# Kernel optimization log

Measured on AMD Instinct MI355X. Metric: run time of the kernel, lower is better.

## Reference

```python
import jax, jax.numpy as jnp
import numpy as np

B, S, D, H, DFF = 4, 2048, 1024, 16, 4096
DK = D // H
EPS = 1e-6


def setup_inputs() -> dict:
    key = jax.random.key(0)
    ks = jax.random.split(key, 8)
    s = 0.02
    return {
        "x": jax.random.normal(ks[0], (B, S, D), jnp.float32),
        "src_mask": jnp.ones((B, 1, 1, S), jnp.int32),
        "w_q": jax.random.normal(ks[1], (D, D), jnp.float32) * s,
        "w_k": jax.random.normal(ks[2], (D, D), jnp.float32) * s,
        "w_v": jax.random.normal(ks[3], (D, D), jnp.float32) * s,
        "w_o": jax.random.normal(ks[4], (D, D), jnp.float32) * s,
        "w1": jax.random.normal(ks[5], (DFF, D), jnp.float32) * s,
        "b1": jnp.zeros((DFF,), jnp.float32),
        "w2": jax.random.normal(ks[6], (D, DFF), jnp.float32) * s,
        "b2": jnp.zeros((D,), jnp.float32),
        "gamma1": jnp.ones((1,), jnp.float32),
        "beta1": jnp.zeros((1,), jnp.float32),
        "gamma2": jnp.ones((1,), jnp.float32),
        "beta2": jnp.zeros((1,), jnp.float32),
    }


def layernorm(x, gamma, beta):
    # matches torch source: unbiased std (ddof=1), eps added to std, scalar gamma/beta
    mean = jnp.mean(x, axis=-1, keepdims=True)
    std = jnp.std(x, axis=-1, keepdims=True, ddof=1)
    return gamma * (x - mean) / (std + EPS) + beta


def mha(x, w_q, w_k, w_v, w_o):
    # Linear(bias=False): y = x @ W.T
    q = (x @ w_q.T).reshape(B, S, H, DK).transpose(0, 2, 1, 3)  # [B,H,S,DK]
    k = (x @ w_k.T).reshape(B, S, H, DK).transpose(0, 2, 1, 3)
    v = (x @ w_v.T).reshape(B, S, H, DK).transpose(0, 2, 1, 3)
    scores = jnp.einsum('bhqd,bhkd->bhqk', q, k) / np.float32(np.sqrt(DK))
    # NOTE: source calls attention.masked_fill(...) without assigning the result,
    # so the mask has no effect; faithfully replicated (mask unused).
    attn = jax.nn.softmax(scores, axis=-1)
    ctx = jnp.einsum('bhqk,bhkd->bhqd', attn, v)  # [B,H,S,DK]
    ctx = ctx.transpose(0, 2, 1, 3).reshape(B, S, D)
    return ctx @ w_o.T


def ffn(x, w1, b1, w2, b2):
    return jax.nn.relu(x @ w1.T + b1) @ w2.T + b2


def reference(x, src_mask, w_q, w_k, w_v, w_o, w1, b1, w2, b2,
              gamma1, beta1, gamma2, beta2):
    # pre-norm residual blocks; dropout is identity in eval
    x = x + mha(layernorm(x, gamma1, beta1), w_q, w_k, w_v, w_o)
    x = x + ffn(layernorm(x, gamma2, beta2), w1, b1, w2, b2)
    return x
```

## Files before the change

kernel.cpp:

```cpp
#include <hip/hip_runtime.h>
#include <hip/hip_bf16.h>

#define DEV static __device__ __forceinline__

typedef unsigned short u16;
typedef float fp32x4 __attribute__((ext_vector_type(4)));
typedef short bf16x8 __attribute__((ext_vector_type(8)));
typedef short bf16x4 __attribute__((ext_vector_type(4)));

DEV float bf2f(u16 u) { return __uint_as_float(((unsigned)u) << 16); }
DEV u16 f2bf(float f) {
  unsigned x = __float_as_uint(f);
  x += 0x7fffu + ((x >> 16) & 1u);
  return (u16)(x >> 16);
}

DEV unsigned cvt_pk_bf16(float a, float b) {
  unsigned r;
  asm("v_cvt_pk_bf16_f32 %0, %1, %2" : "=v"(r) : "v"(a), "v"(b));
  return r;
}

DEV void gload_lds16(const void* g, void* l) {
  __builtin_amdgcn_global_load_lds(
      (__attribute__((address_space(1))) void*)(unsigned long long)g,
      (__attribute__((address_space(3))) void*)(unsigned int)(unsigned long long)l,
      16, 0, 0);
}

__global__ __launch_bounds__(256) void cvt_kernel(const float* __restrict__ in,
                                                  u16* __restrict__ out) {
  const int i = blockIdx.x * 256 + threadIdx.x;
  const fp32x4 v = ((const fp32x4*)in)[i];
  bf16x4 o;
#pragma unroll
  for (int j = 0; j < 4; j++) o[j] = (short)f2bf(v[j]);
  ((bf16x4*)out)[i] = o;
}

__global__ __launch_bounds__(256) void ln_kernel(const float* __restrict__ x,
                                                 u16* __restrict__ y,
                                                 const float* __restrict__ gamma,
                                                 const float* __restrict__ beta) {
  const int row = blockIdx.x;
  const int t = threadIdx.x;
  const fp32x4 v = ((const fp32x4*)(x + (size_t)row * 1024))[t];
  float s = v[0] + v[1] + v[2] + v[3];
  float ss = v[0] * v[0] + v[1] * v[1] + v[2] * v[2] + v[3] * v[3];
#pragma unroll
  for (int o = 32; o > 0; o >>= 1) {
    s += __shfl_down(s, o);
    ss += __shfl_down(ss, o);
  }
  __shared__ float rs[4], rss[4];
  const int w = t >> 6;
  if ((t & 63) == 0) { rs[w] = s; rss[w] = ss; }
  __syncthreads();
  const float S = rs[0] + rs[1] + rs[2] + rs[3];
  const float SS = rss[0] + rss[1] + rss[2] + rss[3];
  const float mean = S * (1.0f / 1024.0f);
  const float var = fmaxf((SS - 1024.0f * mean * mean) * (1.0f / 1023.0f), 0.0f);
  const float sc = gamma[0] / (sqrtf(var) + 1e-6f);
  const float be = beta[0];
  bf16x4 o;
#pragma unroll
  for (int j = 0; j < 4; j++) o[j] = (short)f2bf((v[j] - mean) * sc + be);
  ((bf16x4*)(y + (size_t)row * 1024))[t] = o;
}

template <int EPI>
__global__ __launch_bounds__(256, 2) void gemm_bt(
    const u16* __restrict__ A, const u16* __restrict__ W, u16* __restrict__ Cb,
    float* __restrict__ Cf, const float* __restrict__ bias,
    const float* __restrict__ resid, int M, int N, int K,
    u16* __restrict__ CbK, u16* __restrict__ CbV) {
  __shared__ u16 sA[128 * 32];
  __shared__ u16 sB[128 * 32];
  const int t = threadIdx.x;
  const int lane = t & 63;
  const int w = t >> 6;
  const int wr = (w >> 1) * 64;
  const int wc = (w & 1) * 64;
  const int lr = lane & 15;
  const int hi = lane >> 4;

  const int nwgx = gridDim.x;
  const int orig = blockIdx.y * nwgx + blockIdx.x;
  const int cpx = (nwgx * gridDim.y) >> 3;
  const int logical = (orig & 7) * cpx + (orig >> 3);
  const int bx = logical % nwgx, by = logical / nwgx;

  const u16* gA = A + (size_t)(by * 128 + (t >> 2)) * K + (t & 3) * 8;
  const u16* gB = W + (size_t)(bx * 128 + (t >> 2)) * K + (t & 3) * 8;
  const size_t rstep = (size_t)64 * K;
  u16* lA = &sA[t * 8];
  u16* lB = &sB[t * 8];

  const fp32x4 zero4 = {0.f, 0.f, 0.f, 0.f};
  fp32x4 acc[4][4];
#pragma unroll
  for (int i = 0; i < 4; i++)
#pragma unroll
    for (int j = 0; j < 4; j++) acc[i][j] = zero4;

  for (int k0 = 0; k0 < K; k0 += 32) {
    gload_lds16(gA, lA);
    gload_lds16(gA + rstep, lA + 2048);
    gload_lds16(gB, lB);
    gload_lds16(gB + rstep, lB + 2048);
    gA += 32;
    gB += 32;
    __syncthreads();
    bf16x8 af[4], bfr[4];
#pragma unroll
    for (int i = 0; i < 4; i++)
      af[i] = *(const bf16x8*)&sA[(wr + i * 16 + lr) * 32 + hi * 8];
#pragma unroll
    for (int j = 0; j < 4; j++)
      bfr[j] = *(const bf16x8*)&sB[(wc + j * 16 + lr) * 32 + hi * 8];
#pragma unroll
    for (int i = 0; i < 4; i++)
#pragma unroll
      for (int j = 0; j < 4; j++)
        acc[i][j] =
            __builtin_amdgcn_mfma_f32_16x16x32_bf16(af[i], bfr[j], acc[i][j], 0, 0, 0);
    __syncthreads();
  }

  const int row0 = by * 128 + wr + hi * 4;
  const int col0 = bx * 128 + wc + lr;
  float bj[4] = {0.f, 0.f, 0.f, 0.f};
  if (EPI == 1 || EPI == 3) {
#pragma unroll
    for (int j = 0; j < 4; j++) bj[j] = bias[col0 + j * 16];
  }
  u16* qkvDst = nullptr;
  int colL0 = 0;
  if (EPI == 4) {
    const int sel = col0 >> 10;
    qkvDst = (sel == 0) ? Cb : (sel == 1 ? CbK : CbV);
    colL0 = col0 & 1023;
  }
#pragma unroll
  for (int i = 0; i < 4; i++) {
#pragma unroll
    for (int r = 0; r < 4; r++) {
      const size_t row = (size_t)(row0 + i * 16 + r);
#pragma unroll
      for (int j = 0; j < 4; j++) {
        float v = acc[i][j][r];
        if (EPI == 4) {
          qkvDst[row * 1024 + colL0 + j * 16] = f2bf(v);
          continue;
        }
        const int col = col0 + j * 16;
        if (EPI == 1) v = fmaxf(v + bj[j], 0.f);
        if (EPI == 3) v += bj[j];
        if (EPI >= 2) {
          v += resid[row * N + col];
          Cf[row * N + col] = v;
        } else {
          Cb[row * N + col] = f2bf(v);
        }
      }
    }
  }
}

__global__ __launch_bounds__(256) void vtrans_kernel(const u16* __restrict__ V,
                                                     u16* __restrict__ VT) {
  const int st = blockIdx.x;
  const int h = blockIdx.y;
  const int b = blockIdx.z;
  const int t = threadIdx.x;
  const int r = t >> 2, c0 = (t & 3) * 16;
  __shared__ u16 sT[64][72];

  const u16* src = V + ((size_t)(b * 2048 + st * 64 + r)) * 1024 + h * 64 + c0;
  bf16x8 v0 = *(const bf16x8*)src;
  bf16x8 v1 = *(const bf16x8*)(src + 8);
  const int cb = c0 ^ ((r >> 4) << 4);
  *(bf16x8*)&sT[r][cb] = v0;
  *(bf16x8*)&sT[r][cb + 8] = v1;
  __syncthreads();

  const int dc = r ^ ((c0 >> 4) << 4);
  bf16x8 o0, o1;
#pragma unroll
  for (int i = 0; i < 8; i++) o0[i] = sT[c0 + i][dc];
#pragma unroll
  for (int i = 0; i < 8; i++) o1[i] = sT[c0 + 8 + i][dc];
  u16* dst = VT + ((size_t)((b * 16 + h) * 64 + r)) * 2048 + st * 64 + c0;
  *(bf16x8*)dst = o0;
  *(bf16x8*)(dst + 8) = o1;
}

DEV int swz(int row, int chunk) { return row * 64 + ((chunk ^ (row & 7)) << 3); }

__global__ __launch_bounds__(256, 2) void attn_kernel(const u16* __restrict__ Q,
                                                      const u16* __restrict__ K,
                                                      const u16* __restrict__ VT,
                                                      u16* __restrict__ O) {
  const int orig = blockIdx.x + 32 * (blockIdx.y + 16 * blockIdx.z);
  const int logical = (orig & 7) * 256 + (orig >> 3);
  const int qt = logical & 31;
  const int h = (logical >> 5) & 15;
  const int b = logical >> 9;

  const int t = threadIdx.x, lane = t & 63, w = t >> 6;
  const int lr = lane & 15, hi = lane >> 4;

  __shared__ u16 sK[64 * 64];
  __shared__ u16 sVT[64 * 64];
  __shared__ u16 sQP[64 * 64];

  const size_t base = ((size_t)b * 2048) * 1024 + (size_t)h * 64;
  const size_t vbase = (((size_t)b * 16 + h) * 64) * 2048;
  const int r = t >> 2, c0 = (t & 3) * 16;
  const int wch = (t & 3) * 2;

  {
    const float qs = 0.125f * 1.44269504f;
    const u16* src = Q + base + (size_t)(qt * 64 + r) * 1024 + c0;
    bf16x8 u0 = *(const bf16x8*)src;
    bf16x8 u1 = *(const bf16x8*)(src + 8);
    union { unsigned u[4]; bf16x8 v; } q0, q1;
#pragma unroll
    for (int j = 0; j < 4; j++)
      q0.u[j] = cvt_pk_bf16(bf2f((u16)u0[2 * j]) * qs, bf2f((u16)u0[2 * j + 1]) * qs);
#pragma unroll
    for (int j = 0; j < 4; j++)
      q1.u[j] = cvt_pk_bf16(bf2f((u16)u1[2 * j]) * qs, bf2f((u16)u1[2 * j + 1]) * qs);
    *(bf16x8*)&sQP[swz(r, wch)] = q0.v;
    *(bf16x8*)&sQP[swz(r, wch + 1)] = q1.v;
  }
  __syncthreads();
  const int qrow = w * 16 + lr;
  bf16x8 qreg0 = *(const bf16x8*)&sQP[swz(qrow, hi)];
  bf16x8 qreg1 = *(const bf16x8*)&sQP[swz(qrow, 4 + hi)];

  bf16x8 kA, kB, vA, vB;
  {
    const u16* ks = K + base + (size_t)r * 1024 + c0;
    kA = *(const bf16x8*)ks;
    kB = *(const bf16x8*)(ks + 8);
    const u16* vs = VT + vbase + (size_t)r * 2048 + c0;
    vA = *(const bf16x8*)vs;
    vB = *(const bf16x8*)(vs + 8);
  }

  const fp32x4 zero4 = {0.f, 0.f, 0.f, 0.f};
  fp32x4 onT[4];
#pragma unroll
  for (int df = 0; df < 4; df++) onT[df] = zero4;
  float mrun = -1e30f, lrun = 0.f;

  for (int kt = 0; kt < 32; ++kt) {
    __syncthreads();
    *(bf16x8*)&sK[swz(r, wch)] = kA;
    *(bf16x8*)&sK[swz(r, wch + 1)] = kB;
    *(bf16x8*)&sVT[swz(r, wch)] = vA;
    *(bf16x8*)&sVT[swz(r, wch + 1)] = vB;
    __syncthreads();
    if (kt < 31) {
      const u16* kn = K + base + (size_t)((kt + 1) * 64 + r) * 1024 + c0;
      kA = *(const bf16x8*)kn;
      kB = *(const bf16x8*)(kn + 8);
      const u16* vn = VT + vbase + (size_t)r * 2048 + (kt + 1) * 64 + c0;
      vA = *(const bf16x8*)vn;
      vB = *(const bf16x8*)(vn + 8);
    }

    fp32x4 sc[4];
    __builtin_amdgcn_s_setprio(1);
#pragma unroll
    for (int kk = 0; kk < 4; kk++) {
      fp32x4 a = zero4;
      bf16x8 kf0 = *(const bf16x8*)&sK[swz(kk * 16 + lr, hi)];
      bf16x8 kf1 = *(const bf16x8*)&sK[swz(kk * 16 + lr, 4 + hi)];
      a = __builtin_amdgcn_mfma_f32_16x16x32_bf16(kf0, qreg0, a, 0, 0, 0);
      a = __builtin_amdgcn_mfma_f32_16x16x32_bf16(kf1, qreg1, a, 0, 0, 0);
      sc[kk] = a;
    }
    __builtin_amdgcn_s_setprio(0);

    float m0 = fmaxf(fmaxf(sc[0][0], sc[0][1]), fmaxf(sc[0][2], sc[0][3]));
    float m1 = fmaxf(fmaxf(sc[1][0], sc[1][1]), fmaxf(sc[1][2], sc[1][3]));
    float m2 = fmaxf(fmaxf(sc[2][0], sc[2][1]), fmaxf(sc[2][2], sc[2][3]));
    float m3 = fmaxf(fmaxf(sc[3][0], sc[3][1]), fmaxf(sc[3][2], sc[3][3]));
    float mloc = fmaxf(fmaxf(m0, m1), fmaxf(m2, m3));
    mloc = fmaxf(mloc, __shfl_xor(mloc, 16));
    mloc = fmaxf(mloc, __shfl_xor(mloc, 32));
    if (!__all(mloc - mrun <= 11.0f)) {
      const float mnew = fmaxf(mrun, mloc);
      const float alpha = exp2f(mrun - mnew);
      lrun *= alpha;
#pragma unroll
      for (int df = 0; df < 4; df++) onT[df] *= alpha;
      mrun = mnew;
    }
#pragma unroll
    for (int kk = 0; kk < 4; kk++) {
      float p0 = exp2f(sc[kk][0] - mrun), p1 = exp2f(sc[kk][1] - mrun);
      float p2 = exp2f(sc[kk][2] - mrun), p3 = exp2f(sc[kk][3] - mrun);
      lrun += (p0 + p1) + (p2 + p3);
      uint2 pk = {cvt_pk_bf16(p0, p1), cvt_pk_bf16(p2, p3)};
      *(uint2*)&sQP[swz(qrow, 2 * kk + (hi >> 1)) + (hi & 1) * 4] = pk;
    }

    __builtin_amdgcn_s_setprio(1);
#pragma unroll
    for (int df = 0; df < 4; df++) {
#pragma unroll
      for (int ks = 0; ks < 2; ks++) {
        bf16x8 vf = *(const bf16x8*)&sVT[swz(df * 16 + lr, ks * 4 + hi)];
        bf16x8 pf = *(const bf16x8*)&sQP[swz(qrow, ks * 4 + hi)];
        onT[df] = __builtin_amdgcn_mfma_f32_16x16x32_bf16(vf, pf, onT[df], 0, 0, 0);
      }
    }
    __builtin_amdgcn_s_setprio(0);
  }

  lrun += __shfl_xor(lrun, 16);
  lrun += __shfl_xor(lrun, 32);
  const float invl = 1.0f / lrun;
  u16* dst = O + base + (size_t)(qt * 64 + qrow) * 1024;
#pragma unroll
  for (int df = 0; df < 4; df++) {
    uint2 o2 = {cvt_pk_bf16(onT[df][0] * invl, onT[df][1] * invl),
                cvt_pk_bf16(onT[df][2] * invl, onT[df][3] * invl)};
    *(uint2*)&dst[df * 16 + hi * 4] = o2;
  }
}

extern "C" void kernel_launch(void* const* d_in, const int* in_sizes, int n_in,
                              void* d_out, int out_size, void* d_ws, size_t ws_size,
                              hipStream_t stream) {
  const float* x = (const float*)d_in[0];
  const float* wq = (const float*)d_in[2];
  const float* wk = (const float*)d_in[3];
  const float* wv = (const float*)d_in[4];
  const float* wo = (const float*)d_in[5];
  const float* w1 = (const float*)d_in[6];
  const float* b1 = (const float*)d_in[7];
  const float* w2 = (const float*)d_in[8];
  const float* b2 = (const float*)d_in[9];
  const float* g1 = (const float*)d_in[10];
  const float* be1 = (const float*)d_in[11];
  const float* g2 = (const float*)d_in[12];
  const float* be2 = (const float*)d_in[13];
  float* out = (float*)d_out;

  const size_t MB = 1024ull * 1024ull;
  char* ws = (char*)d_ws;
  if (ws_size < 136 * MB) return;

  u16* wqkv = (u16*)(ws + 0 * MB);
  u16* wqb = (u16*)(ws + 0 * MB);
  u16* wkb = (u16*)(ws + 2 * MB);
  u16* wvb = (u16*)(ws + 4 * MB);
  u16* wob = (u16*)(ws + 6 * MB);
  u16* w1b = (u16*)(ws + 8 * MB);
  u16* w2b = (u16*)(ws + 16 * MB);
  u16* Qb = (u16*)(ws + 24 * MB);
  u16* Kb = (u16*)(ws + 40 * MB);
  u16* Vb = (u16*)(ws + 56 * MB);
  u16* Ctx = (u16*)(ws + 72 * MB);
  u16* Hb = (u16*)(ws + 24 * MB);
  u16* Yb = (u16*)(ws + 88 * MB);
  u16* VTb = (u16*)(ws + 88 * MB);
  float* X2 = (float*)(ws + 104 * MB);

  dim3 blk(256);

  cvt_kernel<<<1024, blk, 0, stream>>>(wq, wqb);
  cvt_kernel<<<1024, blk, 0, stream>>>(wk, wkb);
  cvt_kernel<<<1024, blk, 0, stream>>>(wv, wvb);
  cvt_kernel<<<1024, blk, 0, stream>>>(wo, wob);
  cvt_kernel<<<4096, blk, 0, stream>>>(w1, w1b);
  cvt_kernel<<<4096, blk, 0, stream>>>(w2, w2b);

  ln_kernel<<<8192, blk, 0, stream>>>(x, Yb, g1, be1);

  gemm_bt<4><<<dim3(24, 64), blk, 0, stream>>>(Yb, wqkv, Qb, nullptr, nullptr, nullptr,
                                               8192, 3072, 1024, Kb, Vb);
  vtrans_kernel<<<dim3(32, 16, 4), blk, 0, stream>>>(Vb, VTb);

  attn_kernel<<<dim3(32, 16, 4), blk, 0, stream>>>(Qb, Kb, VTb, Ctx);

  gemm_bt<2><<<dim3(8, 64), blk, 0, stream>>>(Ctx, wob, nullptr, X2, nullptr, x, 8192,
                                              1024, 1024, nullptr, nullptr);

  ln_kernel<<<8192, blk, 0, stream>>>(X2, Yb, g2, be2);

  gemm_bt<1><<<dim3(32, 64), blk, 0, stream>>>(Yb, w1b, Hb, nullptr, b1, nullptr, 8192,
                                               4096, 1024, nullptr, nullptr);

  gemm_bt<3><<<dim3(8, 64), blk, 0, stream>>>(Hb, w2b, nullptr, out, b2, X2, 8192, 1024,
                                              4096, nullptr, nullptr);
}
```

Baseline: 451.2 us.

## Add 256x256 triple-buffered GEMM kernel for QKV and FFN1 projections

Measured after the change: 464.3 us. 2.9% more time.

```diff
diff --git a/kernel.cpp b/kernel.cpp
--- a/kernel.cpp
+++ b/kernel.cpp
@@ -72,8 +72,7 @@
 __global__ __launch_bounds__(256, 2) void gemm_bt(
     const u16* __restrict__ A, const u16* __restrict__ W, u16* __restrict__ Cb,
     float* __restrict__ Cf, const float* __restrict__ bias,
-    const float* __restrict__ resid, int M, int N, int K,
-    u16* __restrict__ CbK, u16* __restrict__ CbV) {
+    const float* __restrict__ resid, int M, int N, int K) {
   __shared__ u16 sA[128 * 32];
   __shared__ u16 sB[128 * 32];
   const int t = threadIdx.x;
@@ -134,13 +133,6 @@
 #pragma unroll
     for (int j = 0; j < 4; j++) bj[j] = bias[col0 + j * 16];
   }
-  u16* qkvDst = nullptr;
-  int colL0 = 0;
-  if (EPI == 4) {
-    const int sel = col0 >> 10;
-    qkvDst = (sel == 0) ? Cb : (sel == 1 ? CbK : CbV);
-    colL0 = col0 & 1023;
-  }
 #pragma unroll
   for (int i = 0; i < 4; i++) {
 #pragma unroll
@@ -148,12 +140,8 @@
       const size_t row = (size_t)(row0 + i * 16 + r);
 #pragma unroll
       for (int j = 0; j < 4; j++) {
+        const int col = col0 + j * 16;
         float v = acc[i][j][r];
-        if (EPI == 4) {
-          qkvDst[row * 1024 + colL0 + j * 16] = f2bf(v);
-          continue;
-        }
-        const int col = col0 + j * 16;
         if (EPI == 1) v = fmaxf(v + bj[j], 0.f);
         if (EPI == 3) v += bj[j];
         if (EPI >= 2) {
@@ -165,6 +153,129 @@
       }
     }
   }
+}
+
+template <int EPI>
+__global__ __launch_bounds__(512, 1) void gemm256(
+    const u16* __restrict__ A, const u16* __restrict__ W, u16* __restrict__ C0,
+    u16* __restrict__ C1, u16* __restrict__ C2, const float* __restrict__ bias,
+    int N, int K) {
+  __shared__ __attribute__((aligned(16))) u16 sA[3][256 * 32];
+  __shared__ __attribute__((aligned(16))) u16 sB[3][256 * 32];
+  const int t = threadIdx.x;
+  const int l = t & 63, wid = t >> 6;
+  const int lr = l & 15, hi = l >> 4;
+  const int wm = wid >> 2, wn = wid & 3;
+
+  const int nwgx = gridDim.x;
+  const int orig = blockIdx.y * nwgx + blockIdx.x;
+  const int cpx = (nwgx * gridDim.y) >> 3;
+  const int logical = (orig & 7) * cpx + (orig >> 3);
+  const int bn = logical % nwgx, bm = logical / nwgx;
+
+  const int rl = l >> 2;
+  const int srcsw = (l & 3) ^ ((l >> 2) & 3) ^ ((l >> 4) & 3);
+  const int rb0 = wid * 16, rb1 = 128 + wid * 16;
+  const u16* gA0 = A + (size_t)(bm * 256 + rb0 + rl) * K + srcsw * 8;
+  const u16* gA1 = A + (size_t)(bm * 256 + rb1 + rl) * K + srcsw * 8;
+  const u16* gB0 = W + (size_t)(bn * 256 + rb0 + rl) * K + srcsw * 8;
+  const u16* gB1 = W + (size_t)(bn * 256 + rb1 + rl) * K + srcsw * 8;
+
+#define STAGE_A(buf, ts)                                      \
+  gload_lds16(gA0 + (ts) * 32, &sA[buf][rb0 * 32 + l * 8]);   \
+  gload_lds16(gA1 + (ts) * 32, &sA[buf][rb1 * 32 + l * 8]);
+#define STAGE_B(buf, ts)                                      \
+  gload_lds16(gB0 + (ts) * 32, &sB[buf][rb0 * 32 + l * 8]);   \
+  gload_lds16(gB1 + (ts) * 32, &sB[buf][rb1 * 32 + l * 8]);
+
+  const int fsw = hi ^ ((lr ^ (lr >> 2)) & 3);
+
+  fp32x4 acc[8][4];
+  const fp32x4 zero4 = {0.f, 0.f, 0.f, 0.f};
+#pragma unroll
+  for (int m = 0; m < 8; m++)
+#pragma unroll
+    for (int n = 0; n < 4; n++) acc[m][n] = zero4;
+
+  STAGE_A(0, 0); STAGE_B(0, 0);
+  STAGE_A(1, 1); STAGE_B(1, 1);
+
+  const int nt = K / 32;
+  for (int tt = 0; tt < nt; ++tt) {
+    const int cur = tt % 3;
+    const int nxt = (tt + 2) % 3;
+    const int ts = (tt + 2) & (nt - 1);
+    asm volatile("s_waitcnt vmcnt(4)" ::: "memory");
+    __builtin_amdgcn_s_barrier();
+
+    bf16x8 bfrag[4], afrag[4];
+#pragma unroll
+    for (int n = 0; n < 4; n++)
+      bfrag[n] = *(const bf16x8*)&sB[cur][(wn * 64 + n * 16 + lr) * 32 + fsw * 8];
+#pragma unroll
+    for (int m = 0; m < 4; m++)
+      afrag[m] = *(const bf16x8*)&sA[cur][(wm * 128 + m * 16 + lr) * 32 + fsw * 8];
+    STAGE_A(nxt, ts);
+    __builtin_amdgcn_s_barrier();
+    __builtin_amdgcn_s_setprio(1);
+#pragma unroll
+    for (int m = 0; m < 4; m++)
+#pragma unroll
+      for (int n = 0; n < 4; n++)
+        acc[m][n] =
+            __builtin_amdgcn_mfma_f32_16x16x32_bf16(afrag[m], bfrag[n], acc[m][n], 0, 0, 0);
+    __builtin_amdgcn_s_setprio(0);
+
+#pragma unroll
+    for (int m = 0; m < 4; m++)
+      afrag[m] =
+          *(const bf16x8*)&sA[cur][(wm * 128 + 64 + m * 16 + lr) * 32 + fsw * 8];
+    STAGE_B(nxt, ts);
+    __builtin_amdgcn_s_barrier();
+    __builtin_amdgcn_s_setprio(1);
+#pragma unroll
+    for (int m = 0; m < 4; m++)
+#pragma unroll
+      for (int n = 0; n < 4; n++)
+        acc[4 + m][n] = __builtin_amdgcn_mfma_f32_16x16x32_bf16(afrag[m], bfrag[n],
+                                                                acc[4 + m][n], 0, 0, 0);
+    __builtin_amdgcn_s_setprio(0);
+  }
+  asm volatile("s_waitcnt vmcnt(0)" ::: "memory");
+
+  const int row0 = bm * 256 + wm * 128 + hi * 4;
+  const int col0 = bn * 256 + wn * 64 + lr;
+  float bj[4] = {0.f, 0.f, 0.f, 0.f};
+  if (EPI == 1) {
+#pragma unroll
+    for (int n = 0; n < 4; n++) bj[n] = bias[col0 + n * 16];
+  }
+  u16* qkvDst = C0;
+  int colL0 = col0;
+  if (EPI == 4) {
+    const int sel = bn >> 2;
+    qkvDst = (sel == 0) ? C0 : (sel == 1 ? C1 : C2);
+    colL0 = col0 & 1023;
+  }
+#pragma unroll
+  for (int m = 0; m < 8; m++) {
+#pragma unroll
+    for (int rr = 0; rr < 4; rr++) {
+      const size_t row = (size_t)(row0 + m * 16 + rr);
+#pragma unroll
+      for (int n = 0; n < 4; n++) {
+        float v = acc[m][n][rr];
+        if (EPI == 1) {
+          v = fmaxf(v + bj[n], 0.f);
+          C0[row * N + col0 + n * 16] = f2bf(v);
+        } else {
+          qkvDst[row * 1024 + colL0 + n * 16] = f2bf(v);
+        }
+      }
+    }
+  }
+#undef STAGE_A
+#undef STAGE_B
 }
 
 __global__ __launch_bounds__(256) void vtrans_kernel(const u16* __restrict__ V,
@@ -382,20 +493,20 @@
 
   ln_kernel<<<8192, blk, 0, stream>>>(x, Yb, g1, be1);
 
-  gemm_bt<4><<<dim3(24, 64), blk, 0, stream>>>(Yb, wqkv, Qb, nullptr, nullptr, nullptr,
-                                               8192, 3072, 1024, Kb, Vb);
+  gemm256<4><<<dim3(12, 32), dim3(512), 0, stream>>>(Yb, wqkv, Qb, Kb, Vb, nullptr,
+                                                     3072, 1024);
   vtrans_kernel<<<dim3(32, 16, 4), blk, 0, stream>>>(Vb, VTb);
 
   attn_kernel<<<dim3(32, 16, 4), blk, 0, stream>>>(Qb, Kb, VTb, Ctx);
 
   gemm_bt<2><<<dim3(8, 64), blk, 0, stream>>>(Ctx, wob, nullptr, X2, nullptr, x, 8192,
-                                              1024, 1024, nullptr, nullptr);
+                                              1024, 1024);
 
   ln_kernel<<<8192, blk, 0, stream>>>(X2, Yb, g2, be2);
 
-  gemm_bt<1><<<dim3(32, 64), blk, 0, stream>>>(Yb, w1b, Hb, nullptr, b1, nullptr, 8192,
-                                               4096, 1024, nullptr, nullptr);
+  gemm256<1><<<dim3(16, 32), dim3(512), 0, stream>>>(Yb, w1b, Hb, nullptr, nullptr, b1,
+                                                     4096, 1024);
 
   gemm_bt<3><<<dim3(8, 64), blk, 0, stream>>>(Hb, w2b, nullptr, out, b2, X2, 8192, 1024,
-                                              4096, nullptr, nullptr);
-}
+                                              4096);
+}
```

## Fuse V transpose into QKV GEMM epilogue and merge weight conversions

Applied to the files above, without the earlier changes.

Measured after the change: 440.3 us (median of 2 runs). -2.4%, faster.

```diff
diff --git a/kernel.cpp b/kernel.cpp
--- a/kernel.cpp
+++ b/kernel.cpp
@@ -28,14 +28,27 @@
       16, 0, 0);
 }
 
-__global__ __launch_bounds__(256) void cvt_kernel(const float* __restrict__ in,
-                                                  u16* __restrict__ out) {
-  const int i = blockIdx.x * 256 + threadIdx.x;
-  const fp32x4 v = ((const fp32x4*)in)[i];
+__global__ __launch_bounds__(256) void cvt_all(
+    const float* __restrict__ wq, const float* __restrict__ wk,
+    const float* __restrict__ wv, const float* __restrict__ wo,
+    const float* __restrict__ w1, const float* __restrict__ w2,
+    u16* __restrict__ dst) {
+  const size_t i = (size_t)blockIdx.x * 256 + threadIdx.x;
+  const size_t e = i * 4;
+  const float* src;
+  size_t off;
+  const size_t M1 = 1u << 20;
+  if (e < M1) { src = wq; off = e; }
+  else if (e < 2 * M1) { src = wk; off = e - M1; }
+  else if (e < 3 * M1) { src = wv; off = e - 2 * M1; }
+  else if (e < 4 * M1) { src = wo; off = e - 3 * M1; }
+  else if (e < 8 * M1) { src = w1; off = e - 4 * M1; }
+  else { src = w2; off = e - 8 * M1; }
+  const fp32x4 v = *(const fp32x4*)(src + off);
   bf16x4 o;
 #pragma unroll
   for (int j = 0; j < 4; j++) o[j] = (short)f2bf(v[j]);
-  ((bf16x4*)out)[i] = o;
+  ((bf16x4*)dst)[i] = o;
 }
 
 __global__ __launch_bounds__(256) void ln_kernel(const float* __restrict__ x,
@@ -129,18 +142,66 @@
 
   const int row0 = by * 128 + wr + hi * 4;
   const int col0 = bx * 128 + wc + lr;
+
+  if constexpr (EPI == 4) {
+    if (col0 < 2048) {
+      u16* qkvDst = (col0 >> 10) ? CbK : Cb;
+      const int colL0 = col0 & 1023;
+#pragma unroll
+      for (int i = 0; i < 4; i++)
+#pragma unroll
+        for (int r = 0; r < 4; r++) {
+          const size_t row = (size_t)(row0 + i * 16 + r);
+#pragma unroll
+          for (int j = 0; j < 4; j++)
+            qkvDst[row * 1024 + colL0 + j * 16] = f2bf(acc[i][j][r]);
+        }
+    } else {
+      __shared__ __attribute__((aligned(16))) u16 sT[2][64 * 72];
+#pragma unroll
+      for (int ph = 0; ph < 2; ++ph) {
+        __syncthreads();
+        if ((w >> 1) == ph) {
+          u16* R = sT[w & 1];
+#pragma unroll
+          for (int j = 0; j < 4; j++) {
+            const int ci = j * 16 + lr;
+            const int X = (ci ^ (ci >> 3)) & 7;
+#pragma unroll
+            for (int i = 0; i < 4; i++)
+#pragma unroll
+              for (int r = 0; r < 4; r++) {
+                const int ri = i * 16 + hi * 4 + r;
+                R[ci * 72 + ((((ri >> 3) ^ X) << 3) | (ri & 7))] =
+                    f2bf(acc[i][j][r]);
+              }
+          }
+        }
+        __syncthreads();
+        if ((w >> 1) == ph) {
+          const u16* R = sT[w & 1];
+          const int ci = lane;
+          const int X = (ci ^ (ci >> 3)) & 7;
+          const int h = (bx - 16) * 2 + (w & 1);
+          const int bidx = by >> 4;
+          const int sb_base = (by & 15) * 128 + (w >> 1) * 64;
+          u16* vdst = CbV + ((size_t)((bidx * 16 + h) * 64 + ci)) * 2048 + sb_base;
+#pragma unroll
+          for (int ch = 0; ch < 8; ch++) {
+            bf16x8 vv = *(const bf16x8*)&R[ci * 72 + ((ch ^ X) << 3)];
+            *(bf16x8*)(vdst + ch * 8) = vv;
+          }
+        }
+      }
+    }
+    return;
+  }
+
   float bj[4] = {0.f, 0.f, 0.f, 0.f};
   if (EPI == 1 || EPI == 3) {
 #pragma unroll
     for (int j = 0; j < 4; j++) bj[j] = bias[col0 + j * 16];
   }
-  u16* qkvDst = nullptr;
-  int colL0 = 0;
-  if (EPI == 4) {
-    const int sel = col0 >> 10;
-    qkvDst = (sel == 0) ? Cb : (sel == 1 ? CbK : CbV);
-    colL0 = col0 & 1023;
-  }
 #pragma unroll
   for (int i = 0; i < 4; i++) {
 #pragma unroll
@@ -148,12 +209,8 @@
       const size_t row = (size_t)(row0 + i * 16 + r);
 #pragma unroll
       for (int j = 0; j < 4; j++) {
+        const int col = col0 + j * 16;
         float v = acc[i][j][r];
-        if (EPI == 4) {
-          qkvDst[row * 1024 + colL0 + j * 16] = f2bf(v);
-          continue;
-        }
-        const int col = col0 + j * 16;
         if (EPI == 1) v = fmaxf(v + bj[j], 0.f);
         if (EPI == 3) v += bj[j];
         if (EPI >= 2) {
@@ -165,34 +222,6 @@
       }
     }
   }
-}
-
-__global__ __launch_bounds__(256) void vtrans_kernel(const u16* __restrict__ V,
-                                                     u16* __restrict__ VT) {
-  const int st = blockIdx.x;
-  const int h = blockIdx.y;
-  const int b = blockIdx.z;
-  const int t = threadIdx.x;
-  const int r = t >> 2, c0 = (t & 3) * 16;
-  __shared__ u16 sT[64][72];
-
-  const u16* src = V + ((size_t)(b * 2048 + st * 64 + r)) * 1024 + h * 64 + c0;
-  bf16x8 v0 = *(const bf16x8*)src;
-  bf16x8 v1 = *(const bf16x8*)(src + 8);
-  const int cb = c0 ^ ((r >> 4) << 4);
-  *(bf16x8*)&sT[r][cb] = v0;
-  *(bf16x8*)&sT[r][cb + 8] = v1;
-  __syncthreads();
-
-  const int dc = r ^ ((c0 >> 4) << 4);
-  bf16x8 o0, o1;
-#pragma unroll
-  for (int i = 0; i < 8; i++) o0[i] = sT[c0 + i][dc];
-#pragma unroll
-  for (int i = 0; i < 8; i++) o1[i] = sT[c0 + 8 + i][dc];
-  u16* dst = VT + ((size_t)((b * 16 + h) * 64 + r)) * 2048 + st * 64 + c0;
-  *(bf16x8*)dst = o0;
-  *(bf16x8*)(dst + 8) = o1;
 }
 
 DEV int swz(int row, int chunk) { return row * 64 + ((chunk ^ (row & 7)) << 3); }
@@ -356,35 +385,25 @@
   if (ws_size < 136 * MB) return;
 
   u16* wqkv = (u16*)(ws + 0 * MB);
-  u16* wqb = (u16*)(ws + 0 * MB);
-  u16* wkb = (u16*)(ws + 2 * MB);
-  u16* wvb = (u16*)(ws + 4 * MB);
   u16* wob = (u16*)(ws + 6 * MB);
   u16* w1b = (u16*)(ws + 8 * MB);
   u16* w2b = (u16*)(ws + 16 * MB);
   u16* Qb = (u16*)(ws + 24 * MB);
   u16* Kb = (u16*)(ws + 40 * MB);
-  u16* Vb = (u16*)(ws + 56 * MB);
+  u16* VTb = (u16*)(ws + 56 * MB);
   u16* Ctx = (u16*)(ws + 72 * MB);
   u16* Hb = (u16*)(ws + 24 * MB);
   u16* Yb = (u16*)(ws + 88 * MB);
-  u16* VTb = (u16*)(ws + 88 * MB);
   float* X2 = (float*)(ws + 104 * MB);
 
   dim3 blk(256);
 
-  cvt_kernel<<<1024, blk, 0, stream>>>(wq, wqb);
-  cvt_kernel<<<1024, blk, 0, stream>>>(wk, wkb);
-  cvt_kernel<<<1024, blk, 0, stream>>>(wv, wvb);
-  cvt_kernel<<<1024, blk, 0, stream>>>(wo, wob);
-  cvt_kernel<<<4096, blk, 0, stream>>>(w1, w1b);
-  cvt_kernel<<<4096, blk, 0, stream>>>(w2, w2b);
+  cvt_all<<<12288, blk, 0, stream>>>(wq, wk, wv, wo, w1, w2, (u16*)ws);
 
   ln_kernel<<<8192, blk, 0, stream>>>(x, Yb, g1, be1);
 
   gemm_bt<4><<<dim3(24, 64), blk, 0, stream>>>(Yb, wqkv, Qb, nullptr, nullptr, nullptr,
-                                               8192, 3072, 1024, Kb, Vb);
-  vtrans_kernel<<<dim3(32, 16, 4), blk, 0, stream>>>(Vb, VTb);
+                                               8192, 3072, 1024, Kb, VTb);
 
   attn_kernel<<<dim3(32, 16, 4), blk, 0, stream>>>(Qb, Kb, VTb, Ctx);
 
```
